# Optimization experiments

Hardware: AMD Instinct MI355X
Metric: run time of the kernel (lower is better)

## Reference

```python
import jax, jax.numpy as jnp
import numpy as np

# S4D (diagonal state space) layer, version=1, bidirectional.
# Faithful to the standard minimal S4D: ZOH-discretized diagonal kernel via
# Vandermonde, causal FFT convolution, D skip, GELU, then 1x1-conv GLU.


def _s4d(u, log_dt, C_re, C_im, log_A_real, A_imag, D_skip, W_glu, b_glu):
    # u: (B, L, H)
    B, L, Hd = u.shape
    dt = jnp.exp(log_dt)                                   # (H,)
    A = -jnp.exp(log_A_real) + 1j * A_imag                 # (H, N2) complex
    dtA = A * dt[:, None]                                  # (H, N2)
    C = (C_re + 1j * C_im) * (jnp.exp(dtA) - 1.0) / A      # (H, N2)
    V = jnp.exp(dtA[:, :, None] * jnp.arange(L))           # (H, N2, L) Vandermonde
    K = 2.0 * jnp.einsum('hn,hnl->hl', C, V).real          # (H, L) SSM kernel
    uT = jnp.swapaxes(u, 1, 2)                             # (B, H, L)
    n = 2 * L                                              # zero-pad for causal conv
    y = jnp.fft.irfft(jnp.fft.rfft(uT, n=n) * jnp.fft.rfft(K, n=n), n=n)[..., :L]
    y = y + uT * D_skip[:, None]                           # skip connection
    y = jax.nn.gelu(y, approximate=False)                  # torch nn.GELU (exact erf)
    # output_linear: Conv1d(H, 2H, 1) + GLU(dim=-2)
    z = jnp.einsum('oh,bhl->bol', W_glu, y) + b_glu[None, :, None]
    y = z[:, :Hd] * jax.nn.sigmoid(z[:, Hd:])
    return jnp.swapaxes(y, 1, 2)                           # (B, L, H)


def setup_inputs() -> dict:
    key = jax.random.key(0)
    B, L, D, N = 64, 2048, 256, 64
    N2 = N // 2
    kx, kf, kr = jax.random.split(key, 3)

    def make_params(k0):
        ks = jax.random.split(k0, 6)
        log_dt = jax.random.uniform(ks[0], (D,)) * (np.log(0.1) - np.log(0.001)) + np.log(0.001)
        C_re = jax.random.normal(ks[1], (D, N2))
        C_im = jax.random.normal(ks[2], (D, N2))
        log_A_real = jnp.log(0.5 * jnp.ones((D, N2), dtype=jnp.float32))
        A_imag = np.pi * jnp.broadcast_to(jnp.arange(N2, dtype=jnp.float32), (D, N2))
        D_skip = jax.random.normal(ks[3], (D,))
        W_glu = jax.random.normal(ks[4], (2 * D, D)) / np.sqrt(D)
        b_glu = jax.random.normal(ks[5], (2 * D,)) * 0.01
        return log_dt, C_re, C_im, log_A_real, A_imag, D_skip, W_glu, b_glu

    pf = make_params(kf)
    pr = make_params(kr)
    names = ['log_dt', 'C_re', 'C_im', 'log_A_real', 'A_imag', 'D_skip', 'W_glu', 'b_glu']
    inp = {'x': jax.random.normal(kx, (B, L, D), dtype=jnp.float32)}
    for n_, v in zip(names, pf):
        inp[n_] = v
    for n_, v in zip(names, pr):
        inp[n_ + '_rev'] = v
    return inp


def reference(x, log_dt, C_re, C_im, log_A_real, A_imag, D_skip, W_glu, b_glu,
              log_dt_rev, C_re_rev, C_im_rev, log_A_real_rev, A_imag_rev,
              D_skip_rev, W_glu_rev, b_glu_rev):
    y_fwd = _s4d(x, log_dt, C_re, C_im, log_A_real, A_imag, D_skip, W_glu, b_glu)
    y_rev = _s4d(x[:, ::-1], log_dt_rev, C_re_rev, C_im_rev, log_A_real_rev,
                 A_imag_rev, D_skip_rev, W_glu_rev, b_glu_rev)
    return y_fwd + y_rev[:, ::-1]
```

## Files before the change

kernel.cpp:

```cpp
#include <hip/hip_runtime.h>
#include <hip/hip_bf16.h>
#include <math.h>

#define Bb 64
#define Ll 2048
#define Hh 256
#define N2v 32
#define NCH 4
#define CLEN (Ll / NCH)

#define WF_OFF 1024
#define BF_OFF 525312
#define GOLD_OFF 529408
#define A2_OFF 529408
#define AF_OFF 4723712
#define WT_OFF 13112320
#define XT_OFF 13243392
#define S_OFF  80352256
#define GT_OFF 214569984
#define WS_NEED 348787712ull
#define GNEW_OFF XT_OFF

typedef __hip_bfloat16 bf16;
typedef float f32x4 __attribute__((ext_vector_type(4)));
typedef _Float16 f16;
typedef _Float16 f16x2 __attribute__((ext_vector_type(2)));
typedef _Float16 f16x4 __attribute__((ext_vector_type(4)));
typedef _Float16 f16x8 __attribute__((ext_vector_type(8)));

__device__ __forceinline__ float b2f(bf16 v) { return __bfloat162float(v); }
__device__ __forceinline__ float ldf(const float* p, int i) { return p[i]; }
__device__ __forceinline__ float ldf(const bf16* p, int i) { return b2f(p[i]); }

__device__ __forceinline__ float4 ld4f(const float* p) { return *(const float4*)p; }
__device__ __forceinline__ float4 ld4f(const bf16* p) {
  ushort4 u = *(const ushort4*)p;
  float4 r;
  r.x = b2f(*(bf16*)&u.x); r.y = b2f(*(bf16*)&u.y);
  r.z = b2f(*(bf16*)&u.z); r.w = b2f(*(bf16*)&u.w);
  return r;
}

__device__ __forceinline__ void gl2lds16(const void* g, void* l) {
  __builtin_amdgcn_global_load_lds((const __attribute__((address_space(1))) void*)g,
                                   (__attribute__((address_space(3))) void*)l, 16, 0, 0);
}

__device__ __forceinline__ f32x4 mfma16(f16x8 a, f16x8 b, f32x4 c) {
  return __builtin_amdgcn_mfma_f32_16x16x32_f16(a, b, c, 0, 0, 0);
}

__device__ __forceinline__ bool input_is_bf16(const void* logA) {
  unsigned u = *(const unsigned*)logA;
  return (u >> 16) == (u & 0xffffu);
}

__global__ void s4d_prep(const void* Wf, const void* bfb, const void* Wr,
                         const void* brb, const void* logA, char* ws) {
  const bool bf = input_is_bf16(logA);
  f16* wdst = (f16*)(ws + WF_OFF);
  float* bdst = (float*)(ws + BF_OFF);
  const int i = blockIdx.x * 256 + threadIdx.x;
  if (i < 262144) {
    const int dstR = i >> 8, k = i & 255;
    const int ht = dstR >> 7, c = dstR & 127;
    const int mat = c >> 5, hl = c & 31;
    const int srow = mat * 256 + ht * 32 + hl;
    const void* src = (srow < 512) ? Wf : Wr;
    const int j = ((srow < 512) ? srow : srow - 512) * 256 + k;
    const float v = bf ? b2f(((const bf16*)src)[j]) : ((const float*)src)[j];
    wdst[i] = (f16)v;
  } else if (i < 262144 + 1024) {
    const int j = i - 262144;
    const void* src = (j < 512) ? bfb : brb;
    const int k = (j < 512) ? j : j - 512;
    bdst[j] = bf ? b2f(((const bf16*)src)[k]) : ((const float*)src)[k];
  }
}

struct ScanP {
  const void* x;
  const void* prm[2][6];
  char* ws;
};

__global__ __launch_bounds__(64) void s4d_prepA(ScanP p) {
  const int d = blockIdx.x >> 8, h = blockIdx.x & 255;
  const int lane = threadIdx.x;
  __shared__ float Ksh[64];
  char* ws = p.ws;
  const bool bf = input_is_bf16(p.prm[0][3]);
#define LDP(w_, i_) (bf ? b2f(((const bf16*)p.prm[d][w_])[i_]) : ((const float*)p.prm[d][w_])[i_])
  const float dt = expf(LDP(0, h));
  const float dsk = LDP(5, h);
  float Kv = 0.f;
  const float dl = (float)lane;
  for (int n = 0; n < 32; ++n) {
    const int idx = h * 32 + n;
    const float Ar = -expf(LDP(3, idx));
    const float Ai = LDP(4, idx);
    const float th = Ai * dt, rr = Ar * dt;
    const float er = expf(rr);
    const float wr = er * cosf(th), wi = er * sinf(th);
    const float den = 1.f / (Ar * Ar + Ai * Ai);
    const float Er = wr - 1.f, Ei = wi;
    const float qr = (Er * Ar + Ei * Ai) * den, qi = (Ei * Ar - Er * Ai) * den;
    const float CR = LDP(1, idx), CI = LDP(2, idx);
    const float cre = 2.f * (CR * qr - CI * qi), cim = 2.f * (CR * qi + CI * qr);
    const float pe = expf(rr * dl), pang = th * dl;
    Kv += cre * pe * cosf(pang) - cim * pe * sinf(pang);
  }
  Ksh[lane] = Kv;
  if (lane < 32) {
    const int idx = h * 32 + lane;
    const float Ar = -expf(LDP(3, idx));
    const float Ai = LDP(4, idx);
    const float th = Ai * dt, rr = Ar * dt;
    const float e64 = expf(rr * 64.f);
    float2 wt;
    wt.x = e64 * cosf(th * 64.f);
    wt.y = e64 * sinf(th * 64.f);
    ((float2*)(ws + WT_OFF))[(d * 256 + h) * 32 + lane] = wt;
  }
  __syncthreads();
  f16* arow = (f16*)(ws + AF_OFF) + ((size_t)(d * 256 + h) * 64 + lane) * 128;
  for (int j = 0; j < 64; ++j) {
    float v = 0.f;
    if (d == 0) { if (j <= lane) v = Ksh[lane - j]; }
    else        { if (j >= lane) v = Ksh[j - lane]; }
    if (j == lane) v += dsk;
    arow[j] = (f16)v;
  }
  const float pexp = (d == 0) ? (float)(lane + 1) : (float)(64 - lane);
  for (int n = 0; n < 32; ++n) {
    const int idx = h * 32 + n;
    const float Ar = -expf(LDP(3, idx));
    const float Ai = LDP(4, idx);
    const float th = Ai * dt, rr = Ar * dt;
    const float er = expf(rr);
    const float wr = er * cosf(th), wi = er * sinf(th);
    const float den = 1.f / (Ar * Ar + Ai * Ai);
    const float Er = wr - 1.f, Ei = wi;
    const float qr = (Er * Ar + Ei * Ai) * den, qi = (Ei * Ar - Er * Ai) * den;
    const float CR = LDP(1, idx), CI = LDP(2, idx);
    const float cre = 2.f * (CR * qr - CI * qi), cim = 2.f * (CR * qi + CI * qr);
    const float pe = expf(rr * pexp), pang = th * pexp;
    const float pwr = pe * cosf(pang), pwi = pe * sinf(pang);
    arow[64 + 2 * n]     = (f16)(cre * pwr - cim * pwi);
    arow[64 + 2 * n + 1] = (f16)(-(cre * pwi + cim * pwr));
  }
  {
    const int n = lane >> 1, im = lane & 1;
    const int idx = h * 32 + n;
    const float Ar = -expf(LDP(3, idx));
    const float Ai = LDP(4, idx);
    const float th = Ai * dt, rr = Ar * dt;
    f16* a2 = (f16*)(ws + A2_OFF) + ((size_t)h * 128 + d * 64 + lane) * 64;
    for (int i = 0; i < 64; ++i) {
      const float pp = (d == 0) ? (float)(63 - i) : (float)i;
      const float e = expf(rr * pp), ang = th * pp;
      a2[i] = (f16)(im ? e * sinf(ang) : e * cosf(ang));
    }
  }
#undef LDP
}

template <typename T>
__device__ __forceinline__ void t1_body(const T* __restrict__ x, char* ws, float* tile) {
  const int b = blockIdx.x, h0 = blockIdx.y * 64;
  const int t = threadIdx.x;
  f16* xT = (f16*)(ws + XT_OFF);
  const int h4r = (t & 15) * 4;
  const int lrb = t >> 4;
  const int hw = t & 63;
  const int lo = t >> 6;
  const int lbase = blockIdx.z * 512;
  for (int l0 = lbase; l0 < lbase + 512; l0 += 64) {
    __syncthreads();
#pragma unroll
    for (int p = 0; p < 4; ++p) {
      const int l = p * 16 + lrb;
      const float4 v = ld4f(x + ((size_t)b * 2048 + l0 + l) * 256 + h0 + h4r);
      *(float4*)&tile[l * 68 + h4r] = v;
    }
    __syncthreads();
    f16x8 o0, o1;
#pragma unroll
    for (int j = 0; j < 8; ++j) o0[j] = (f16)tile[(lo * 16 + j) * 68 + hw];
#pragma unroll
    for (int j = 0; j < 8; ++j) o1[j] = (f16)tile[(lo * 16 + 8 + j) * 68 + hw];
    f16* dst = xT + ((size_t)(h0 + hw) * 64 + b) * 2048 + l0 + lo * 16;
    *(f16x8*)dst = o0;
    *(f16x8*)(dst + 8) = o1;
  }
}

__global__ __launch_bounds__(256) void s4d_t1(const void* x, const void* logA, char* ws) {
  __shared__ float tile[64 * 68];
  if (input_is_bf16(logA)) t1_body<bf16>((const bf16*)x, ws, tile);
  else                     t1_body<float>((const float*)x, ws, tile);
}

__global__ __launch_bounds__(256, 3) void s4d_krs(char* __restrict__ ws) {
  __shared__ char lds[34816];
  const int bid = blockIdx.x;
  const int h = ((bid >> 7) << 3) | (bid & 7);
  const int cb = (bid >> 3) & 15;
  const int t = threadIdx.x, lane = t & 63, wave = t >> 6;
  const int lm = lane & 15, lq = lane >> 4;
  const f16* xT = (const f16*)(ws + XT_OFF);
  const char* a2b = ws + A2_OFF + (size_t)h * 128 * 64 * 2;
  const int srow = lane >> 3;
  const int sch = (lane & 7) ^ srow;
#pragma unroll
  for (int j = 0; j < 4; ++j) {
    const int rb = wave * 4 + j;
    const int r = rb * 8 + srow;
    gl2lds16(a2b + r * 128 + sch * 16, lds + rb * 1024);
    const int col = cb * 128 + r;
    const int b_ = col >> 5, c_ = col & 31;
    gl2lds16((const char*)(xT + ((size_t)(h * 64 + b_) * 2048 + c_ * 64)) + sch * 16,
             lds + 16384 + rb * 1024);
  }
  __syncthreads();
  f32x4 acc[2][8];
#pragma unroll
  for (int i = 0; i < 2; ++i)
#pragma unroll
    for (int j = 0; j < 8; ++j) acc[i][j] = (f32x4){0.f, 0.f, 0.f, 0.f};
#pragma unroll
  for (int kb = 0; kb < 2; ++kb) {
    const int cA = kb * 4 + lq;
    f16x8 au[2], a2f[8];
#pragma unroll
    for (int i = 0; i < 2; ++i) {
      const int r = wave * 32 + i * 16 + lm;
      au[i] = *(const f16x8*)(lds + 16384 + r * 128 + ((cA ^ (r & 7)) * 16));
    }
#pragma unroll
    for (int j = 0; j < 8; ++j) {
      const int r = j * 16 + lm;
      a2f[j] = *(const f16x8*)(lds + r * 128 + ((cA ^ (r & 7)) * 16));
    }
#pragma unroll
    for (int i = 0; i < 2; ++i)
#pragma unroll
      for (int j = 0; j < 8; ++j) acc[i][j] = mfma16(au[i], a2f[j], acc[i][j]);
  }
  __syncthreads();
  f16* Cl = (f16*)lds;
#pragma unroll
  for (int i = 0; i < 2; ++i)
#pragma unroll
    for (int j = 0; j < 8; ++j)
#pragma unroll
      for (int r = 0; r < 4; ++r)
        Cl[(wave * 32 + i * 16 + lq * 4 + r) * 136 + j * 16 + lm] = (f16)acc[i][j][r];
  __syncthreads();
  const int n = t & 31, dir = (t >> 5) & 1, bl = wave;
  const float2 wt = ((const float2*)(ws + WT_OFF))[(dir * 256 + h) * 32 + n];
  f16* Sg = (f16*)(ws + S_OFF) + ((size_t)h * 2048 + cb * 128 + bl * 32) * 128 + dir * 64 + 2 * n;
  const f16* Cr = Cl + (size_t)(bl * 32) * 136 + dir * 64 + 2 * n;
  float sr = 0.f, si = 0.f;
  const int c0 = dir ? 31 : 0, cstep = dir ? -1 : 1;
  for (int it = 0; it < 32; ++it) {
    const int c = c0 + it * cstep;
    f16x2 sv; sv[0] = (f16)sr; sv[1] = (f16)si;
    *(f16x2*)(Sg + (size_t)c * 128) = sv;
    const float rr = (float)Cr[c * 136], ri = (float)Cr[c * 136 + 1];
    const float a = sr;
    sr = wt.x * a - wt.y * si + rr;
    si = wt.x * si + wt.y * a + ri;
  }
}

__global__ __launch_bounds__(256, 2) void s4d_k3(char* __restrict__ ws) {
  __shared__ char lds[57344];
  const int bid = blockIdx.x;
  const int h = ((bid >> 8) << 3) | (bid & 7);
  const int cb = (bid >> 3) & 31;
  const int t = threadIdx.x, lane = t & 63, wave = t >> 6;
  const int lm = lane & 15, lq = lane >> 4;
  const f16* xT = (const f16*)(ws + XT_OFF);
  const char* afb = ws + AF_OFF + (size_t)h * 64 * 128 * 2;
  const char* arb = ws + AF_OFF + (size_t)(256 + h) * 64 * 128 * 2;
  const char* sb = ws + S_OFF;
  {
    const int sr4 = lane >> 4, c16 = lane & 15;
#pragma unroll
    for (int j = 0; j < 4; ++j) {
      const int rb = wave * 4 + j;
      const int r = rb * 4 + sr4;
      const int sc = c16 ^ (r & 7);
      gl2lds16(afb + r * 256 + sc * 16, lds + rb * 1024);
      gl2lds16(arb + r * 256 + sc * 16, lds + 16384 + rb * 1024);
    }
  }
  {
    const int sr8 = lane >> 3, c8 = lane & 7;
#pragma unroll
    for (int j = 0; j < 2; ++j) {
      const int rb = wave * 2 + j;
      const int clr = rb * 8 + sr8;
      const int col = cb * 64 + clr;
      const int b_ = col >> 5, c_ = col & 31;
      const int sc = c8 ^ (clr & 7);
      gl2lds16((const char*)(xT + ((size_t)(h * 64 + b_) * 2048 + c_ * 64)) + sc * 16,
               lds + 32768 + rb * 1024);
      const char* srow = sb + ((size_t)h * 2048 + col) * 256;
      gl2lds16(srow + sc * 16,       lds + 40960 + rb * 1024);
      gl2lds16(srow + 128 + sc * 16, lds + 49152 + rb * 1024);
    }
  }
  __syncthreads();
  const int dir = wave >> 1, chf = wave & 1;
  const char* At = lds + dir * 16384;
  f32x4 acc[4][2];
#pragma unroll
  for (int i = 0; i < 4; ++i)
#pragma unroll
    for (int j = 0; j < 2; ++j) acc[i][j] = (f32x4){0.f, 0.f, 0.f, 0.f};
#pragma unroll
  for (int kb = 0; kb < 4; ++kb) {
    f16x8 av[4], bv[2];
    const int cA = kb * 4 + lq;
#pragma unroll
    for (int i = 0; i < 4; ++i) {
      const int r = i * 16 + lm;
      av[i] = *(const f16x8*)(At + r * 256 + ((cA ^ (r & 7)) * 16));
    }
    const char* Bt = lds + 32768 + ((kb < 2) ? 0 : (dir ? 16384 : 8192));
    const int cB = (kb & 1) * 4 + lq;
#pragma unroll
    for (int j = 0; j < 2; ++j) {
      const int r = chf * 32 + j * 16 + lm;
      bv[j] = *(const f16x8*)(Bt + r * 128 + ((cB ^ (r & 7)) * 16));
    }
#pragma unroll
    for (int i = 0; i < 4; ++i)
#pragma unroll
      for (int j = 0; j < 2; ++j) acc[i][j] = mfma16(av[i], bv[j], acc[i][j]);
  }
  f16* gT = (f16*)(ws + GT_OFF);
#pragma unroll
  for (int i = 0; i < 4; ++i)
#pragma unroll
    for (int j = 0; j < 2; ++j) {
      const int col = cb * 64 + chf * 32 + j * 16 + lm;
      const int b_ = col >> 5, c_ = col & 31;
      const int i0 = i * 16 + lq * 4;
      f16x4 o;
#pragma unroll
      for (int r = 0; r < 4; ++r) {
        const float y = acc[i][j][r];
        o[r] = (f16)(0.5f * y * (1.f + erff(y * 0.70710678118654752f)));
      }
      *(f16x4*)(gT + ((size_t)((dir * 256 + h) * 64 + b_)) * 2048 + c_ * 64 + i0) = o;
    }
}

__global__ __launch_bounds__(256) void s4d_tr(char* __restrict__ ws) {
  __shared__ f16 tile[32 * 80];
  const int bid = blockIdx.x;
  const int hq = bid & 7, b = (bid >> 3) & 63, dir = bid >> 9;
  const int t = threadIdx.x;
  const int hb = hq * 32;
  const f16* gT = (const f16*)(ws + GT_OFF);
  f16* gm = (f16*)(ws + GNEW_OFF) + (size_t)dir * ((size_t)Bb * Ll * Hh);
  const int hl = t >> 3, lg = t & 7;
  const int lw = t >> 2, hc = t & 3;
  const f16* grow = gT + ((size_t)((dir * 256 + hb + hl) * 64 + b)) * 2048 + lg * 8;
  for (int l0 = 0; l0 < 2048; l0 += 64) {
    __syncthreads();
    *(f16x8*)&tile[hl * 80 + lg * 8] = *(const f16x8*)(grow + l0);
    __syncthreads();
    ushort us[8];
#pragma unroll
    for (int e = 0; e < 8; ++e)
      us[e] = *(const ushort*)&tile[(hc * 8 + e) * 80 + lw];
    uint4 o;
    o.x = (unsigned)us[0] | ((unsigned)us[1] << 16);
    o.y = (unsigned)us[2] | ((unsigned)us[3] << 16);
    o.z = (unsigned)us[4] | ((unsigned)us[5] << 16);
    o.w = (unsigned)us[6] | ((unsigned)us[7] << 16);
    *(uint4*)((char*)gm + ((size_t)b * 2048 + l0 + lw) * 512 + (hb + hc * 8) * 2) = o;
  }
}

template <typename T>
__device__ __forceinline__ void scan_body(
    const T* __restrict__ x, const T* ldt_p, const T* cre_p, const T* cim_p,
    const T* lar_p, const T* aim_p, const T* dsk_p, f16* gbase, float2* S) {
  const int t = threadIdx.x;
  const int lane = t & 63;
  const int ch = t >> 6;
  const int hloc = lane & 7;
  const int ngrp = lane >> 3;
  const int b = blockIdx.x;
  const int hblk = blockIdx.y;
  const int dir = blockIdx.z;
  const int h = hblk * 8 + hloc;

  const float dt = expf(ldf(ldt_p, h));
  float wre[4], wim[4], cre[4], cim[4], sre[4], sim[4];
#pragma unroll
  for (int j = 0; j < 4; ++j) {
    const int idx = h * N2v + ngrp * 4 + j;
    const float Ar = -expf(ldf(lar_p, idx));
    const float Ai = ldf(aim_p, idx);
    const float er = expf(Ar * dt);
    const float wr = er * cosf(Ai * dt), wi = er * sinf(Ai * dt);
    wre[j] = wr; wim[j] = wi;
    const float Er = wr - 1.0f, Ei = wi;
    const float den = 1.0f / (Ar * Ar + Ai * Ai);
    const float qr = (Er * Ar + Ei * Ai) * den;
    const float qi = (Ei * Ar - Er * Ai) * den;
    const float CR = ldf(cre_p, idx);
    const float CI = ldf(cim_p, idx);
    cre[j] = 2.0f * (CR * qr - CI * qi);
    cim[j] = 2.0f * (CR * qi + CI * qr);
    sre[j] = 0.0f; sim[j] = 0.0f;
  }
  const float dsk = ldf(dsk_p, h);

  const int base = b * (Ll * Hh) + h;
  const int stride = dir ? -Hh : Hh;
  const T* x0 = x + base + (dir ? (Ll - 1) * Hh : 0);
  f16* g0 = gbase + dir * (Bb * Ll * Hh) + base + (dir ? (Ll - 1) * Hh : 0);

  if (ch < NCH - 1) {
    const T* xp = x0 + ch * CLEN * stride;
    for (int it = 0; it < CLEN / 4; ++it) {
      const float u0 = ldf(xp, 0);
      const float u1 = ldf(xp, stride);
      const float u2 = ldf(xp, 2 * stride);
      const float u3 = ldf(xp, 3 * stride);
      xp += 4 * stride;
#pragma unroll
      for (int k = 0; k < 4; ++k) {
        const float U = (k == 0) ? u0 : (k == 1) ? u1 : (k == 2) ? u2 : u3;
#pragma unroll
        for (int j = 0; j < 4; ++j) {
          const float a = sre[j], bb = sim[j];
          sre[j] = fmaf(wre[j], a, fmaf(-wim[j], bb, U));
          sim[j] = fmaf(wre[j], bb, wim[j] * a);
        }
      }
    }
#pragma unroll
    for (int j = 0; j < 4; ++j)
      S[((ch * 8 + ngrp) * 4 + j) * 8 + hloc] = (float2){sre[j], sim[j]};
  }
  __syncthreads();

  float pr[4], pi[4];
#pragma unroll
  for (int j = 0; j < 4; ++j) { pr[j] = wre[j]; pi[j] = wim[j]; }
  for (int q = 0; q < 9; ++q) {
#pragma unroll
    for (int j = 0; j < 4; ++j) {
      const float a = pr[j], bb = pi[j];
      pr[j] = fmaf(a, a, -bb * bb);
      pi[j] = 2.0f * a * bb;
    }
  }
#pragma unroll
  for (int j = 0; j < 4; ++j) { sre[j] = 0.0f; sim[j] = 0.0f; }
  for (int cc = 0; cc < ch; ++cc) {
#pragma unroll
    for (int j = 0; j < 4; ++j) {
      const float2 sv = S[((cc * 8 + ngrp) * 4 + j) * 8 + hloc];
      const float a = sre[j], bb = sim[j];
      sre[j] = fmaf(pr[j], a, fmaf(-pi[j], bb, sv.x));
      sim[j] = fmaf(pr[j], bb, fmaf(pi[j], a, sv.y));
    }
  }

  const T* xp = x0 + ch * CLEN * stride;
  f16* gp = g0 + ch * CLEN * stride;
  const bool q0 = (ngrp & 1) != 0;
  const bool q1 = (ngrp & 2) != 0;
  const bool q2 = (ngrp & 4) != 0;
  for (int it = 0; it < CLEN / 8; ++it) {
    float u[8], P[8];
#pragma unroll
    for (int k = 0; k < 8; ++k) u[k] = ldf(xp, k * stride);
    xp += 8 * stride;
#pragma unroll
    for (int k = 0; k < 8; ++k) {
      float pa = 0.0f, pb = 0.0f;
#pragma unroll
      for (int j = 0; j < 4; ++j) {
        const float a = sre[j], bb = sim[j];
        sre[j] = fmaf(wre[j], a, fmaf(-wim[j], bb, u[k]));
        sim[j] = fmaf(wre[j], bb, wim[j] * a);
        pa = fmaf(cre[j], sre[j], pa);
        pb = fmaf(cim[j], sim[j], pb);
      }
      P[k] = pa - pb;
    }
    const float Q0 = (q0 ? P[1] : P[0]) + __shfl_xor(q0 ? P[0] : P[1], 8);
    const float Q1 = (q0 ? P[3] : P[2]) + __shfl_xor(q0 ? P[2] : P[3], 8);
    const float Q2 = (q0 ? P[5] : P[4]) + __shfl_xor(q0 ? P[4] : P[5], 8);
    const float Q3 = (q0 ? P[7] : P[6]) + __shfl_xor(q0 ? P[6] : P[7], 8);
    const float R0 = (q1 ? Q1 : Q0) + __shfl_xor(q1 ? Q0 : Q1, 16);
    const float R1 = (q1 ? Q3 : Q2) + __shfl_xor(q1 ? Q2 : Q3, 16);
    const float Tt = (q2 ? R1 : R0) + __shfl_xor(q2 ? R0 : R1, 32);
    const float s01 = q0 ? u[1] : u[0];
    const float s23 = q0 ? u[3] : u[2];
    const float s45 = q0 ? u[5] : u[4];
    const float s67 = q0 ? u[7] : u[6];
    const float Uo = q2 ? (q1 ? s67 : s45) : (q1 ? s23 : s01);
    const float y = fmaf(dsk, Uo, Tt);
    const float ge = 0.5f * y * (1.0f + erff(y * 0.70710678118654752f));
    gp[ngrp * stride] = (f16)ge;
    gp += 8 * stride;
  }
}

__global__ __launch_bounds__(256) void s4d_scan(ScanP p) {
  __shared__ float2 S[(NCH - 1) * 8 * 4 * 8];
  const int dir = blockIdx.z;
  f16* g = (f16*)(p.ws + GOLD_OFF);
  if (input_is_bf16(p.prm[0][3])) {
    scan_body<bf16>((const bf16*)p.x, (const bf16*)p.prm[dir][0],
                    (const bf16*)p.prm[dir][1], (const bf16*)p.prm[dir][2],
                    (const bf16*)p.prm[dir][3], (const bf16*)p.prm[dir][4],
                    (const bf16*)p.prm[dir][5], g, S);
  } else {
    scan_body<float>((const float*)p.x, (const float*)p.prm[dir][0],
                     (const float*)p.prm[dir][1], (const float*)p.prm[dir][2],
                     (const float*)p.prm[dir][3], (const float*)p.prm[dir][4],
                     (const float*)p.prm[dir][5], g, S);
  }
}

__global__ __launch_bounds__(256, 3) void s4d_glu_gemm(const char* __restrict__ ws,
                                                       void* __restrict__ out_v,
                                                       const void* logA,
                                                       unsigned goff) {
  __shared__ char lds[49152];
  const bool obf = input_is_bf16(logA);
  const char* gf = ws + goff;
  const char* gr = gf + (size_t)Bb * Ll * Hh * 2;
  const char* wre = ws + WF_OFF;
  const float* bias = (const float*)(ws + BF_OFF);

  const int lane = threadIdx.x & 63;
  const int wave = threadIdx.x >> 6;
  const int lm = lane & 15;
  const int lq = lane >> 4;
  const int bid = blockIdx.x;
  const int mt = ((bid >> 6) << 3) | (bid & 7);
  const int ht = (bid >> 3) & 7;
  const size_t mrow0 = (size_t)mt * 128;

  f32x4 acc[4][4];
#pragma unroll
  for (int i = 0; i < 4; ++i)
#pragma unroll
    for (int ct = 0; ct < 4; ++ct) acc[i][ct] = (f32x4){0.f, 0.f, 0.f, 0.f};

  const int srow16 = lane >> 2;
  const int chunk = (lane & 3) ^ ((srow16 & 3) ^ ((srow16 >> 2) & 3));
  const char* gsrc[6];
  unsigned ldst[6];
#pragma unroll
  for (int j = 0; j < 6; ++j) {
    const int s_ = wave * 6 + j;
    const int tile_ = s_ >> 3;
    const int rb_ = s_ & 7;
    const int row_ = rb_ * 16 + srow16;
    const char* base;
    if (tile_ == 0)      base = gf + (mrow0 + row_) * 512;
    else if (tile_ == 1) base = gr + (mrow0 + row_) * 512;
    else                 base = wre + (size_t)(ht * 128 + row_) * 512;
    gsrc[j] = base + chunk * 16;
    ldst[j] = tile_ * 8192 + rb_ * 1024;
  }

#define STAGE2(BUFI, KS2)                                                \
  do {                                                                   \
    _Pragma("unroll")                                                    \
    for (int j_ = 0; j_ < 6; ++j_)                                       \
      gl2lds16(gsrc[j_] + (KS2) * 64, lds + (BUFI) * 24576 + ldst[j_]);  \
  } while (0)

  STAGE2(0, 0);
#pragma unroll
  for (int ks = 0; ks < 8; ++ks) {
    const int buf = ks & 1;
    if (ks < 7) {
      STAGE2(buf ^ 1, ks + 1);
      asm volatile("s_waitcnt vmcnt(6)" ::: "memory");
    } else {
      asm volatile("s_waitcnt vmcnt(0)" ::: "memory");
    }
    __builtin_amdgcn_s_barrier();
    __builtin_amdgcn_sched_barrier(0);
    const char* Ab = lds + buf * 24576 + ((wave >> 1) ? 8192 : 0);
    const char* Bt = lds + buf * 24576 + 16384;
    f16x8 af[4], bf_[4];
#pragma unroll
    for (int i = 0; i < 4; ++i) {
      const int r = (wave & 1) * 64 + i * 16 + lm;
      const int sw = (r & 3) ^ ((r >> 2) & 3);
      af[i] = *(const f16x8*)(Ab + r * 64 + ((lq ^ sw) * 16));
    }
#pragma unroll
    for (int ct = 0; ct < 4; ++ct) {
      const int r = (wave >> 1) * 64 + ct * 16 + lm;
      const int sw = (r & 3) ^ ((r >> 2) & 3);
      bf_[ct] = *(const f16x8*)(Bt + r * 64 + ((lq ^ sw) * 16));
    }
    __builtin_amdgcn_s_setprio(1);
#pragma unroll
    for (int i = 0; i < 4; ++i)
#pragma unroll
      for (int ct = 0; ct < 4; ++ct)
        acc[i][ct] = mfma16(af[i], bf_[ct], acc[i][ct]);
    __builtin_amdgcn_s_setprio(0);
    __builtin_amdgcn_sched_barrier(0);
    __builtin_amdgcn_s_barrier();
    __builtin_amdgcn_sched_barrier(0);
  }
#undef STAGE2

  __syncthreads();
  float* xb = (float*)lds;
  if (wave >= 2) {
#pragma unroll
    for (int ctl = 0; ctl < 2; ++ctl) {
      const float blo = bias[512 + ht * 32 + ctl * 16 + lm];
      const float bhi = bias[768 + ht * 32 + ctl * 16 + lm];
#pragma unroll
      for (int i = 0; i < 4; ++i)
#pragma unroll
        for (int r = 0; r < 4; ++r) {
          const float z3 = acc[i][ctl][r] + blo;
          const float z4 = acc[i][ctl + 2][r] + bhi;
          xb[(((wave & 1) * 2 + ctl) * 16 + i * 4 + r) * 64 + lane] =
              z3 * (1.0f / (1.0f + expf(-z4)));
        }
    }
  }
  __syncthreads();
  if (wave < 2) {
#pragma unroll
    for (int ctl = 0; ctl < 2; ++ctl) {
      const int hout = ht * 32 + ctl * 16 + lm;
      const float blo = bias[hout];
      const float bhi = bias[256 + hout];
#pragma unroll
      for (int i = 0; i < 4; ++i)
#pragma unroll
        for (int r = 0; r < 4; ++r) {
          const float z1 = acc[i][ctl][r] + blo;
          const float z2 = acc[i][ctl + 2][r] + bhi;
          const float v = z1 * (1.0f / (1.0f + expf(-z2))) +
                          xb[(((wave & 1) * 2 + ctl) * 16 + i * 4 + r) * 64 + lane];
          const size_t m = mrow0 + (wave & 1) * 64 + i * 16 + lq * 4 + r;
          if (obf) ((bf16*)out_v)[m * Hh + hout] = __float2bfloat16(v);
          else     ((float*)out_v)[m * Hh + hout] = v;
        }
    }
  }
}

extern "C" void kernel_launch(void* const* d_in, const int* in_sizes, int n_in,
                              void* d_out, int out_size, void* d_ws, size_t ws_size,
                              hipStream_t stream) {
  ScanP p;
  p.x = d_in[0];
  for (int d = 0; d < 2; ++d)
    for (int j = 0; j < 6; ++j) p.prm[d][j] = d_in[1 + d * 8 + j];
  p.ws = (char*)d_ws;

  hipLaunchKernelGGL(s4d_prep, dim3(1028), dim3(256), 0, stream,
                     d_in[7], d_in[8], d_in[15], d_in[16], d_in[4], (char*)d_ws);

  if (ws_size >= (size_t)WS_NEED) {
    hipLaunchKernelGGL(s4d_prepA, dim3(512), dim3(64), 0, stream, p);
    hipLaunchKernelGGL(s4d_t1, dim3(64, 4, 4), dim3(256), 0, stream,
                       d_in[0], d_in[4], (char*)d_ws);
    hipLaunchKernelGGL(s4d_krs, dim3(4096), dim3(256), 0, stream, (char*)d_ws);
    hipLaunchKernelGGL(s4d_k3, dim3(8192), dim3(256), 0, stream, (char*)d_ws);
    hipLaunchKernelGGL(s4d_tr, dim3(1024), dim3(256), 0, stream, (char*)d_ws);
    hipLaunchKernelGGL(s4d_glu_gemm, dim3(8192), dim3(256), 0, stream,
                       (const char*)d_ws, d_out, d_in[4], (unsigned)GNEW_OFF);
  } else {
    hipLaunchKernelGGL(s4d_scan, dim3(Bb, Hh / 8, 2), dim3(256), 0, stream, p);
    hipLaunchKernelGGL(s4d_glu_gemm, dim3(8192), dim3(256), 0, stream,
                       (const char*)d_ws, d_out, d_in[4], (unsigned)GOLD_OFF);
  }
}
```

Baseline: 749.8 us.

## Fuse chunk-state scan kernel and intra-chunk GEMM into one kernel via LDS

Merges the chunk-reduction/state-scan kernel (krs) with the output GEMM kernel (k3) so the per-chunk carried states stay in LDS instead of being written to and reread from a large global S buffer. The A-factor loads are issued early and overlapped with the first GEMM and scan using explicit waitcnt and barriers. Each block now covers 128 columns, with a larger accumulator tile. In exchange, LDS use grows to about 130KB per block, occupancy drops to one block per CU, and the serial scan is no longer hidden by other resident blocks.

```diff
diff --git a/kernel.cpp b/kernel.cpp
--- a/kernel.cpp
+++ b/kernel.cpp
@@ -16,7 +16,6 @@
 #define AF_OFF 4723712
 #define WT_OFF 13112320
 #define XT_OFF 13243392
-#define S_OFF  80352256
 #define GT_OFF 214569984
 #define WS_NEED 348787712ull
 #define GNEW_OFF XT_OFF
@@ -201,8 +200,8 @@
   else                     t1_body<float>((const float*)x, ws, tile);
 }
 
-__global__ __launch_bounds__(256, 3) void s4d_krs(char* __restrict__ ws) {
-  __shared__ char lds[34816];
+__global__ __launch_bounds__(256, 1) void s4d_kf(char* __restrict__ ws) {
+  __shared__ char lds[133120];
   const int bid = blockIdx.x;
   const int h = ((bid >> 7) << 3) | (bid & 7);
   const int cb = (bid >> 3) & 15;
@@ -210,152 +209,154 @@
   const int lm = lane & 15, lq = lane >> 4;
   const f16* xT = (const f16*)(ws + XT_OFF);
   const char* a2b = ws + A2_OFF + (size_t)h * 128 * 64 * 2;
-  const int srow = lane >> 3;
-  const int sch = (lane & 7) ^ srow;
-#pragma unroll
-  for (int j = 0; j < 4; ++j) {
-    const int rb = wave * 4 + j;
-    const int r = rb * 8 + srow;
-    gl2lds16(a2b + r * 128 + sch * 16, lds + rb * 1024);
-    const int col = cb * 128 + r;
-    const int b_ = col >> 5, c_ = col & 31;
-    gl2lds16((const char*)(xT + ((size_t)(h * 64 + b_) * 2048 + c_ * 64)) + sch * 16,
-             lds + 16384 + rb * 1024);
-  }
-  __syncthreads();
-  f32x4 acc[2][8];
-#pragma unroll
-  for (int i = 0; i < 2; ++i)
-#pragma unroll
-    for (int j = 0; j < 8; ++j) acc[i][j] = (f32x4){0.f, 0.f, 0.f, 0.f};
-#pragma unroll
-  for (int kb = 0; kb < 2; ++kb) {
-    const int cA = kb * 4 + lq;
-    f16x8 au[2], a2f[8];
-#pragma unroll
-    for (int i = 0; i < 2; ++i) {
-      const int r = wave * 32 + i * 16 + lm;
-      au[i] = *(const f16x8*)(lds + 16384 + r * 128 + ((cA ^ (r & 7)) * 16));
-    }
-#pragma unroll
-    for (int j = 0; j < 8; ++j) {
-      const int r = j * 16 + lm;
-      a2f[j] = *(const f16x8*)(lds + r * 128 + ((cA ^ (r & 7)) * 16));
-    }
-#pragma unroll
-    for (int i = 0; i < 2; ++i)
-#pragma unroll
-      for (int j = 0; j < 8; ++j) acc[i][j] = mfma16(au[i], a2f[j], acc[i][j]);
-  }
-  __syncthreads();
-  f16* Cl = (f16*)lds;
-#pragma unroll
-  for (int i = 0; i < 2; ++i)
-#pragma unroll
-    for (int j = 0; j < 8; ++j)
-#pragma unroll
-      for (int r = 0; r < 4; ++r)
-        Cl[(wave * 32 + i * 16 + lq * 4 + r) * 136 + j * 16 + lm] = (f16)acc[i][j][r];
-  __syncthreads();
-  const int n = t & 31, dir = (t >> 5) & 1, bl = wave;
-  const float2 wt = ((const float2*)(ws + WT_OFF))[(dir * 256 + h) * 32 + n];
-  f16* Sg = (f16*)(ws + S_OFF) + ((size_t)h * 2048 + cb * 128 + bl * 32) * 128 + dir * 64 + 2 * n;
-  const f16* Cr = Cl + (size_t)(bl * 32) * 136 + dir * 64 + 2 * n;
-  float sr = 0.f, si = 0.f;
-  const int c0 = dir ? 31 : 0, cstep = dir ? -1 : 1;
-  for (int it = 0; it < 32; ++it) {
-    const int c = c0 + it * cstep;
-    f16x2 sv; sv[0] = (f16)sr; sv[1] = (f16)si;
-    *(f16x2*)(Sg + (size_t)c * 128) = sv;
-    const float rr = (float)Cr[c * 136], ri = (float)Cr[c * 136 + 1];
-    const float a = sr;
-    sr = wt.x * a - wt.y * si + rr;
-    si = wt.x * si + wt.y * a + ri;
-  }
-}
-
-__global__ __launch_bounds__(256, 2) void s4d_k3(char* __restrict__ ws) {
-  __shared__ char lds[57344];
-  const int bid = blockIdx.x;
-  const int h = ((bid >> 8) << 3) | (bid & 7);
-  const int cb = (bid >> 3) & 31;
-  const int t = threadIdx.x, lane = t & 63, wave = t >> 6;
-  const int lm = lane & 15, lq = lane >> 4;
-  const f16* xT = (const f16*)(ws + XT_OFF);
   const char* afb = ws + AF_OFF + (size_t)h * 64 * 128 * 2;
   const char* arb = ws + AF_OFF + (size_t)(256 + h) * 64 * 128 * 2;
-  const char* sb = ws + S_OFF;
+
   {
+    const int srow = lane >> 3;
+    const int sch = (lane & 7) ^ srow;
+#pragma unroll
+    for (int j = 0; j < 4; ++j) {
+      const int rb = wave * 4 + j;
+      const int r = rb * 8 + srow;
+      gl2lds16(a2b + r * 128 + sch * 16, lds + rb * 1024);
+      const int col = cb * 128 + r;
+      const int b_ = col >> 5, c_ = col & 31;
+      gl2lds16((const char*)(xT + ((size_t)(h * 64 + b_) * 2048 + c_ * 64)) + sch * 16,
+               lds + 16384 + rb * 1024);
+    }
     const int sr4 = lane >> 4, c16 = lane & 15;
 #pragma unroll
     for (int j = 0; j < 4; ++j) {
       const int rb = wave * 4 + j;
       const int r = rb * 4 + sr4;
       const int sc = c16 ^ (r & 7);
-      gl2lds16(afb + r * 256 + sc * 16, lds + rb * 1024);
-      gl2lds16(arb + r * 256 + sc * 16, lds + 16384 + rb * 1024);
-    }
-  }
+      gl2lds16(afb + r * 256 + sc * 16, lds + 32768 + rb * 1024);
+      gl2lds16(arb + r * 256 + sc * 16, lds + 49152 + rb * 1024);
+    }
+  }
+  asm volatile("s_waitcnt vmcnt(8)" ::: "memory");
+  __builtin_amdgcn_s_barrier();
+  __builtin_amdgcn_sched_barrier(0);
+
   {
-    const int sr8 = lane >> 3, c8 = lane & 7;
-#pragma unroll
-    for (int j = 0; j < 2; ++j) {
-      const int rb = wave * 2 + j;
-      const int clr = rb * 8 + sr8;
-      const int col = cb * 64 + clr;
-      const int b_ = col >> 5, c_ = col & 31;
-      const int sc = c8 ^ (clr & 7);
-      gl2lds16((const char*)(xT + ((size_t)(h * 64 + b_) * 2048 + c_ * 64)) + sc * 16,
-               lds + 32768 + rb * 1024);
-      const char* srow = sb + ((size_t)h * 2048 + col) * 256;
-      gl2lds16(srow + sc * 16,       lds + 40960 + rb * 1024);
-      gl2lds16(srow + 128 + sc * 16, lds + 49152 + rb * 1024);
-    }
-  }
-  __syncthreads();
-  const int dir = wave >> 1, chf = wave & 1;
-  const char* At = lds + dir * 16384;
-  f32x4 acc[4][2];
+    f32x4 acc[2][8];
+#pragma unroll
+    for (int i = 0; i < 2; ++i)
+#pragma unroll
+      for (int j = 0; j < 8; ++j) acc[i][j] = (f32x4){0.f, 0.f, 0.f, 0.f};
+#pragma unroll
+    for (int kb = 0; kb < 2; ++kb) {
+      const int cA = kb * 4 + lq;
+      f16x8 au[2], a2f[8];
+#pragma unroll
+      for (int i = 0; i < 2; ++i) {
+        const int r = wave * 32 + i * 16 + lm;
+        au[i] = *(const f16x8*)(lds + 16384 + r * 128 + ((cA ^ (r & 7)) * 16));
+      }
+#pragma unroll
+      for (int j = 0; j < 8; ++j) {
+        const int r = j * 16 + lm;
+        a2f[j] = *(const f16x8*)(lds + r * 128 + ((cA ^ (r & 7)) * 16));
+      }
+#pragma unroll
+      for (int i = 0; i < 2; ++i)
+#pragma unroll
+        for (int j = 0; j < 8; ++j) acc[i][j] = mfma16(au[i], a2f[j], acc[i][j]);
+    }
+    f16* Cl = (f16*)(lds + 65536);
+#pragma unroll
+    for (int i = 0; i < 2; ++i)
+#pragma unroll
+      for (int j = 0; j < 8; ++j)
+#pragma unroll
+        for (int r = 0; r < 4; ++r)
+          Cl[(wave * 32 + i * 16 + lq * 4 + r) * 136 + j * 16 + lm] = (f16)acc[i][j][r];
+  }
+  asm volatile("s_waitcnt lgkmcnt(0)" ::: "memory");
+  __builtin_amdgcn_sched_barrier(0);
+
+  {
+    const int n = t & 31, dirn = (t >> 5) & 1, bl = wave;
+    const float2 wt = ((const float2*)(ws + WT_OFF))[(dirn * 256 + h) * 32 + n];
+    unsigned cv[32];
+    const char* Crb = lds + 65536 + (size_t)(bl * 32) * 272 + dirn * 128 + 4 * n;
+#pragma unroll
+    for (int c = 0; c < 32; ++c) cv[c] = *(const unsigned*)(Crb + c * 272);
+    float sr = 0.f, si = 0.f;
+    char* Sb = lds + 100352 + dirn * 128 + 4 * (n & 3);
+    const int cc0 = n >> 2;
+    const int rbase = bl * 32;
+#define SCAN_STEP(c_)                                                         \
+    {                                                                         \
+      const int r_ = rbase + (c_);                                            \
+      f16x2 sv; sv[0] = (f16)sr; sv[1] = (f16)si;                             \
+      *(f16x2*)(Sb + (size_t)r_ * 256 + ((cc0 ^ ((c_) & 7)) * 16)) = sv;      \
+      const f16x2 cvv = *(const f16x2*)&cv[c_];                               \
+      const float rr_ = (float)cvv[0], ri_ = (float)cvv[1];                   \
+      const float a_ = sr;                                                    \
+      sr = wt.x * a_ - wt.y * si + rr_;                                       \
+      si = wt.x * si + wt.y * a_ + ri_;                                       \
+    }
+    if (dirn == 0) {
+#pragma unroll
+      for (int c = 0; c < 32; ++c) SCAN_STEP(c)
+    } else {
+#pragma unroll
+      for (int i2 = 0; i2 < 32; ++i2) { const int c = 31 - i2; SCAN_STEP(c) }
+    }
+#undef SCAN_STEP
+  }
+  asm volatile("s_waitcnt vmcnt(0) lgkmcnt(0)" ::: "memory");
+  __builtin_amdgcn_s_barrier();
+  __builtin_amdgcn_sched_barrier(0);
+
+  const int dir2 = wave >> 1, ch2 = wave & 1;
+  const char* At = lds + 32768 + dir2 * 16384;
+  f32x4 acc2[4][4];
 #pragma unroll
   for (int i = 0; i < 4; ++i)
 #pragma unroll
-    for (int j = 0; j < 2; ++j) acc[i][j] = (f32x4){0.f, 0.f, 0.f, 0.f};
+    for (int ct = 0; ct < 4; ++ct) acc2[i][ct] = (f32x4){0.f, 0.f, 0.f, 0.f};
 #pragma unroll
   for (int kb = 0; kb < 4; ++kb) {
-    f16x8 av[4], bv[2];
     const int cA = kb * 4 + lq;
+    const int cB = (kb & 1) * 4 + lq;
+    f16x8 av[4], bv[4];
 #pragma unroll
     for (int i = 0; i < 4; ++i) {
       const int r = i * 16 + lm;
       av[i] = *(const f16x8*)(At + r * 256 + ((cA ^ (r & 7)) * 16));
     }
-    const char* Bt = lds + 32768 + ((kb < 2) ? 0 : (dir ? 16384 : 8192));
-    const int cB = (kb & 1) * 4 + lq;
-#pragma unroll
-    for (int j = 0; j < 2; ++j) {
-      const int r = chf * 32 + j * 16 + lm;
-      bv[j] = *(const f16x8*)(Bt + r * 128 + ((cB ^ (r & 7)) * 16));
+#pragma unroll
+    for (int ct = 0; ct < 4; ++ct) {
+      const int r = ch2 * 64 + ct * 16 + lm;
+      if (kb < 2)
+        bv[ct] = *(const f16x8*)(lds + 16384 + r * 128 + ((cB ^ (r & 7)) * 16));
+      else
+        bv[ct] = *(const f16x8*)(lds + 100352 + (size_t)r * 256 + dir2 * 128 +
+                                 ((cB ^ (r & 7)) * 16));
     }
 #pragma unroll
     for (int i = 0; i < 4; ++i)
 #pragma unroll
-      for (int j = 0; j < 2; ++j) acc[i][j] = mfma16(av[i], bv[j], acc[i][j]);
+      for (int ct = 0; ct < 4; ++ct) acc2[i][ct] = mfma16(av[i], bv[ct], acc2[i][ct]);
   }
   f16* gT = (f16*)(ws + GT_OFF);
 #pragma unroll
   for (int i = 0; i < 4; ++i)
 #pragma unroll
-    for (int j = 0; j < 2; ++j) {
-      const int col = cb * 64 + chf * 32 + j * 16 + lm;
+    for (int ct = 0; ct < 4; ++ct) {
+      const int col = cb * 128 + ch2 * 64 + ct * 16 + lm;
       const int b_ = col >> 5, c_ = col & 31;
       const int i0 = i * 16 + lq * 4;
       f16x4 o;
 #pragma unroll
       for (int r = 0; r < 4; ++r) {
-        const float y = acc[i][j][r];
+        const float y = acc2[i][ct][r];
         o[r] = (f16)(0.5f * y * (1.f + erff(y * 0.70710678118654752f)));
       }
-      *(f16x4*)(gT + ((size_t)((dir * 256 + h) * 64 + b_)) * 2048 + c_ * 64 + i0) = o;
+      *(f16x4*)(gT + ((size_t)((dir2 * 256 + h) * 64 + b_)) * 2048 + c_ * 64 + i0) = o;
     }
 }
 
@@ -683,8 +684,7 @@
     hipLaunchKernelGGL(s4d_prepA, dim3(512), dim3(64), 0, stream, p);
     hipLaunchKernelGGL(s4d_t1, dim3(64, 4, 4), dim3(256), 0, stream,
                        d_in[0], d_in[4], (char*)d_ws);
-    hipLaunchKernelGGL(s4d_krs, dim3(4096), dim3(256), 0, stream, (char*)d_ws);
-    hipLaunchKernelGGL(s4d_k3, dim3(8192), dim3(256), 0, stream, (char*)d_ws);
+    hipLaunchKernelGGL(s4d_kf, dim3(4096), dim3(256), 0, stream, (char*)d_ws);
     hipLaunchKernelGGL(s4d_tr, dim3(1024), dim3(256), 0, stream, (char*)d_ws);
     hipLaunchKernelGGL(s4d_glu_gemm, dim3(8192), dim3(256), 0, stream,
                        (const char*)d_ws, d_out, d_in[4], (unsigned)GNEW_OFF);
```

New measurement: 790.7 us. 1.05x slower.
